# Performance work log

Measured on AMD Instinct MI355X. Metric: run time of the kernel, lower is better.

The kernel has to match this reference:

```python
import jax, jax.numpy as jnp
import numpy as np

B, T, C, H, HS = 4, 2048, 1024, 16, 64
EPS = 1e-5


def setup_inputs() -> dict:
    key = jax.random.key(0)
    ks = jax.random.split(key, 16)
    s = lambda k, shp, fan: jax.random.normal(k, shp, jnp.float32) * (fan ** -0.5)
    return {
        "x": jax.random.normal(ks[0], (B, T, C), jnp.float32),
        "wq": s(ks[1], (H, C, HS), C), "bq": jnp.zeros((H, HS), jnp.float32),
        "wk": s(ks[2], (H, C, HS), C), "bk": jnp.zeros((H, HS), jnp.float32),
        "wv": s(ks[3], (H, C, HS), C), "bv": jnp.zeros((H, HS), jnp.float32),
        "wp": s(ks[4], (C, C), C), "bp": jnp.zeros((C,), jnp.float32),
        "w1": s(ks[5], (C, 4 * C), C), "b1": jnp.zeros((4 * C,), jnp.float32),
        "w2": s(ks[6], (4 * C, C), 4 * C), "b2": jnp.zeros((C,), jnp.float32),
        "g1": jnp.ones((C,), jnp.float32), "be1": jnp.zeros((C,), jnp.float32),
        "g2": jnp.ones((C,), jnp.float32), "be2": jnp.zeros((C,), jnp.float32),
    }


def _layernorm(x, g, b):
    mu = jnp.mean(x, axis=-1, keepdims=True)
    var = jnp.mean(jnp.square(x - mu), axis=-1, keepdims=True)
    return (x - mu) * jax.lax.rsqrt(var + EPS) * g + b


def reference(x, wq, bq, wk, bk, wv, bv, wp, bp, w1, b1, w2, b2, g1, be1, g2, be2):
    Bc, Tc, Cc = x.shape
    h = _layernorm(x, g1, be1)
    # per-head projections stacked: [B,H,T,HS]
    q = jnp.einsum('btc,hcd->bhtd', h, wq) + bq[None, :, None, :]
    k = jnp.einsum('btc,hcd->bhtd', h, wk) + bk[None, :, None, :]
    v = jnp.einsum('btc,hcd->bhtd', h, wv) + bv[None, :, None, :]
    # NOTE: source scales by 1/sqrt(n_embd), not 1/sqrt(head_size)
    scores = jnp.einsum('bhtd,bhsd->bhts', q, k) * (Cc ** -0.5)
    causal = jnp.tril(jnp.ones((Tc, Tc), bool))
    scores = jnp.where(causal, scores, -jnp.inf)
    attn = jax.nn.softmax(scores, axis=-1)
    out = jnp.einsum('bhts,bhsd->bhtd', attn, v)
    out = out.transpose(0, 2, 1, 3).reshape(Bc, Tc, Cc)  # concat heads
    x = x + out @ wp + bp
    h2 = _layernorm(x, g2, be2)
    ffn = jax.nn.relu(h2 @ w1 + b1) @ w2 + b2
    return x + ffn
```

## Files before the change

kernel.cpp:

```cpp
#include <hip/hip_runtime.h>


constexpr int Bb = 4, Tt = 2048, Cc = 1024, Hh = 16, HSz = 64, Ff = 4096;
constexpr int Mrows = Bb * Tt;

typedef __attribute__((ext_vector_type(8))) short bf16x8;
typedef __attribute__((ext_vector_type(4))) float f32x4;

__device__ __forceinline__ ushort f2bf(float f) {
  uint u = __builtin_bit_cast(uint, f);
  uint r = (u + 0x7fffu + ((u >> 16) & 1u)) >> 16;
  return (ushort)r;
}
__device__ __forceinline__ float bf2f(ushort s) {
  return __builtin_bit_cast(float, ((uint)s) << 16);
}
__device__ __forceinline__ uint cvtpk_bf16(float lo, float hi) {
  uint r;
  asm("v_cvt_pk_bf16_f32 %0, %1, %2" : "=v"(r) : "v"(lo), "v"(hi));
  return r;
}
__device__ __forceinline__ void gload16(const void* g, void* l) {
  __builtin_amdgcn_global_load_lds(
      (const __attribute__((address_space(1))) void*)g,
      (__attribute__((address_space(3))) void*)l, 16, 0, 0);
}

__global__ __launch_bounds__(256) void ln_kernel(const float* __restrict__ x,
                                                 const float* __restrict__ g,
                                                 const float* __restrict__ b,
                                                 ushort* __restrict__ out) {
  int row = blockIdx.x;
  const float* xr = x + (size_t)row * Cc;
  int c4 = threadIdx.x * 4;
  float4 v = *(const float4*)(xr + c4);
  float s1 = v.x + v.y + v.z + v.w;
  float s2 = v.x * v.x + v.y * v.y + v.z * v.z + v.w * v.w;
#pragma unroll
  for (int off = 32; off >= 1; off >>= 1) {
    s1 += __shfl_xor(s1, off);
    s2 += __shfl_xor(s2, off);
  }
  __shared__ float red[8];
  int wid = threadIdx.x >> 6, lane = threadIdx.x & 63;
  if (lane == 0) { red[wid] = s1; red[4 + wid] = s2; }
  __syncthreads();
  float t1 = red[0] + red[1] + red[2] + red[3];
  float t2 = red[4] + red[5] + red[6] + red[7];
  float mu = t1 * (1.0f / Cc);
  float var = t2 * (1.0f / Cc) - mu * mu;
  float rs = rsqrtf(var + 1e-5f);
  float4 gv = *(const float4*)(g + c4);
  float4 bv = *(const float4*)(b + c4);
  ushort4 o;
  o.x = f2bf((v.x - mu) * rs * gv.x + bv.x);
  o.y = f2bf((v.y - mu) * rs * gv.y + bv.y);
  o.z = f2bf((v.z - mu) * rs * gv.z + bv.z);
  o.w = f2bf((v.w - mu) * rs * gv.w + bv.w);
  *(ushort4*)(out + (size_t)row * Cc + c4) = o;
}

__device__ __forceinline__ void tcast_body(const float* __restrict__ src,
                                           ushort* __restrict__ dst, int ldS,
                                           int ldD, int r0, int c0) {
  __shared__ float t[32][33];
  int c = threadIdx.x & 31, r8 = threadIdx.x >> 5;
#pragma unroll
  for (int i = 0; i < 4; ++i) {
    int r = r8 + i * 8;
    t[r][c] = src[(size_t)(r0 + r) * ldS + c0 + c];
  }
  __syncthreads();
#pragma unroll
  for (int i = 0; i < 4; ++i) {
    int rr = r8 + i * 8;
    dst[(size_t)(c0 + rr) * ldD + r0 + c] = f2bf(t[c][rr]);
  }
}

__global__ __launch_bounds__(256) void tcast_kernel(const float* __restrict__ src,
                                                    ushort* __restrict__ dst,
                                                    int ldS, int ldD) {
  tcast_body(src, dst, ldS, ldD, blockIdx.x * 32, blockIdx.y * 32);
}

__global__ __launch_bounds__(256) void tcast_qkv(const float* __restrict__ wq,
                                                 const float* __restrict__ wk,
                                                 const float* __restrict__ wv,
                                                 ushort* __restrict__ dst) {
  int z = blockIdx.z, zz = z >> 4, h = z & 15;
  const float* src = (zz == 0 ? wq : (zz == 1 ? wk : wv)) + (size_t)h * Cc * HSz;
  ushort* d = dst + (size_t)(zz * 1024 + h * 64) * 1024;
  tcast_body(src, d, HSz, Cc, blockIdx.x * 32, blockIdx.y * 32);
}

__global__ __launch_bounds__(256) void bias_concat(const float* __restrict__ bq,
                                                   const float* __restrict__ bk,
                                                   const float* __restrict__ bv,
                                                   float* __restrict__ dst) {
  int i = blockIdx.x * 256 + threadIdx.x;
  dst[i] = i < 1024 ? bq[i] : (i < 2048 ? bk[i - 1024] : bv[i - 2048]);
}

__device__ __forceinline__ void gemm_main(const ushort* __restrict__ A, int lda,
                                          const ushort* __restrict__ Bt, int ldb,
                                          int K, int m0, int n0,
                                          ushort* __restrict__ As,
                                          ushort* __restrict__ Bs,
                                          f32x4 (&acc)[4][2]) {
  int tid = threadIdx.x, wid = tid >> 6, lane = tid & 63;
  int wr = wid >> 2, wc = wid & 3, fr = lane & 15, fq = lane >> 4;
  const ushort* Ag = A + (size_t)m0 * lda;
  const ushort* Bg = Bt + (size_t)n0 * ldb;
  for (int k0 = 0; k0 < K; k0 += 64) {
#pragma unroll
    for (int c = 0; c < 2; ++c) {
      int slot = c * 512 + tid;
      int row = slot >> 3, s = slot & 7;
      int sw = (s << 3) ^ ((row & 7) << 3);
      gload16(Ag + (size_t)row * lda + k0 + sw, As + (size_t)(c * 512 + wid * 64) * 8);
      gload16(Bg + (size_t)row * ldb + k0 + sw, Bs + (size_t)(c * 512 + wid * 64) * 8);
    }
    __syncthreads();
    bf16x8 av[4][2], bv[2][2];
#pragma unroll
    for (int m = 0; m < 4; ++m) {
      int row = wr * 64 + m * 16 + fr;
#pragma unroll
      for (int ks = 0; ks < 2; ++ks)
        av[m][ks] = *(const bf16x8*)&As[row * 64 + (((ks * 4 + fq) ^ (row & 7)) << 3)];
    }
#pragma unroll
    for (int n = 0; n < 2; ++n) {
      int row = wc * 32 + n * 16 + fr;
#pragma unroll
      for (int ks = 0; ks < 2; ++ks)
        bv[n][ks] = *(const bf16x8*)&Bs[row * 64 + (((ks * 4 + fq) ^ (row & 7)) << 3)];
    }
#pragma unroll
    for (int m = 0; m < 4; ++m)
#pragma unroll
      for (int n = 0; n < 2; ++n)
#pragma unroll
        for (int ks = 0; ks < 2; ++ks)
          acc[m][n] = __builtin_amdgcn_mfma_f32_16x16x32_bf16(
              av[m][ks], bv[n][ks], acc[m][n], 0, 0, 0);
    __syncthreads();
  }
}

__device__ __forceinline__ void xcd_swz(int& bx, int& by) {
  int bid = blockIdx.x + blockIdx.y * gridDim.x;
  int cpx = (gridDim.x * gridDim.y) >> 3;
  int id = (bid & 7) * cpx + (bid >> 3);
  bx = id % gridDim.x;
  by = id / gridDim.x;
}

template <bool RELU, bool HASRES, bool OUTBF16>
__global__ __launch_bounds__(512) void gemm_bf16(
    const ushort* __restrict__ A, int lda, const ushort* __restrict__ Bt,
    int ldb, const float* __restrict__ bias, const float* __restrict__ res,
    void* __restrict__ Cout, int ldc, int K) {
  __shared__ __align__(16) ushort As[128 * 64];
  __shared__ __align__(16) ushort Bs[128 * 64];
  f32x4 acc[4][2] = {};
  int bx, by;
  xcd_swz(bx, by);
  int m0 = by * 128, n0 = bx * 128;
  gemm_main(A, lda, Bt, ldb, K, m0, n0, As, Bs, acc);
  int lane = threadIdx.x & 63, wid = threadIdx.x >> 6;
  int wr = wid >> 2, wc = wid & 3, fr = lane & 15, fq = lane >> 4;
#pragma unroll
  for (int m = 0; m < 4; ++m) {
    int gm = m0 + wr * 64 + m * 16 + fq * 4;
#pragma unroll
    for (int n = 0; n < 2; ++n) {
      int gn = n0 + wc * 32 + n * 16 + fr;
      float bsv = bias[gn];
#pragma unroll
      for (int j = 0; j < 4; ++j) {
        int row = gm + j;
        float v = acc[m][n][j] + bsv;
        if constexpr (HASRES) v += res[(size_t)row * ldc + gn];
        if constexpr (RELU) v = fmaxf(v, 0.f);
        if constexpr (OUTBF16)
          ((ushort*)Cout)[(size_t)row * ldc + gn] = f2bf(v);
        else
          ((float*)Cout)[(size_t)row * ldc + gn] = v;
      }
    }
  }
}

__global__ __launch_bounds__(512) void gemm_qkv(const ushort* __restrict__ A,
                                                const ushort* __restrict__ Bt,
                                                const float* __restrict__ bias,
                                                ushort* __restrict__ q,
                                                ushort* __restrict__ k,
                                                ushort* __restrict__ vt) {
  __shared__ __align__(16) ushort As[128 * 64];
  __shared__ __align__(16) ushort Bs[128 * 64];
  f32x4 acc[4][2] = {};
  int bx, by;
  xcd_swz(bx, by);
  int m0 = by * 128, n0 = bx * 128;
  gemm_main(A, 1024, Bt, 1024, 1024, m0, n0, As, Bs, acc);
  int lane = threadIdx.x & 63, wid = threadIdx.x >> 6;
  int wr = wid >> 2, wc = wid & 3, fr = lane & 15, fq = lane >> 4;
  const float qscale = 1.4426950408889634f / 32.0f;
#pragma unroll
  for (int m = 0; m < 4; ++m) {
    int gm = m0 + wr * 64 + m * 16 + fq * 4;
#pragma unroll
    for (int n = 0; n < 2; ++n) {
      int gn = n0 + wc * 32 + n * 16 + fr;
      float bsv = bias[gn];
      if (gn < 1024) {
#pragma unroll
        for (int j = 0; j < 4; ++j)
          q[(size_t)(gm + j) * 1024 + gn] = f2bf((acc[m][n][j] + bsv) * qscale);
      } else if (gn < 2048) {
        int col = gn - 1024;
#pragma unroll
        for (int j = 0; j < 4; ++j)
          k[(size_t)(gm + j) * 1024 + col] = f2bf(acc[m][n][j] + bsv);
      } else {
        int dd = gn - 2048, h = dd >> 6, d = dd & 63;
        int bbr = gm >> 11, t = gm & 2047;
        ushort4 pw = {f2bf(acc[m][n][0] + bsv), f2bf(acc[m][n][1] + bsv),
                      f2bf(acc[m][n][2] + bsv), f2bf(acc[m][n][3] + bsv)};
        *(ushort4*)&vt[(((size_t)(bbr * 16 + h)) * 64 + d) * 2048 + t] = pw;
      }
    }
  }
}

constexpr int QB = 128, KVB = 64;
__global__ __launch_bounds__(256) void attn_kernel(const ushort* __restrict__ Qb,
                                                   const ushort* __restrict__ Kb,
                                                   const ushort* __restrict__ Vt,
                                                   ushort* __restrict__ att) {
  __shared__ __align__(16) ushort Klds[64 * 64];
  __shared__ __align__(16) ushort Vlds[64 * 64];
  __shared__ __align__(16) ushort Plds[4][32 * 64];
  int tid = threadIdx.x, wid = tid >> 6, lane = tid & 63;
  int fr = lane & 15, fq = lane >> 4;
  int bh = blockIdx.y, bb = bh >> 4, hh = bh & 15;
  const ushort* qkbase = Qb + ((size_t)bb * Tt) * Cc + hh * HSz;
  const ushort* Kbase = Kb + ((size_t)bb * Tt) * Cc + hh * HSz;
  const ushort* Vbase = Vt + ((size_t)(bb * Hh + hh)) * HSz * Tt;

#pragma unroll 1
  for (int pass = 0; pass < 2; ++pass) {
    int qt = pass ? (Tt / QB - 1 - (int)blockIdx.x) : (int)blockIdx.x;
    int q0 = qt * QB;
    int q0w = q0 + wid * 32;

    bf16x8 Qreg[2][2];
#pragma unroll
    for (int qs = 0; qs < 2; ++qs)
#pragma unroll
      for (int d2 = 0; d2 < 2; ++d2)
        Qreg[qs][d2] = *(const bf16x8*)(qkbase +
            (size_t)(q0w + qs * 16 + fr) * Cc + d2 * 32 + fq * 8);
    f32x4 Oa[2][4] = {};
    float mrow[2] = {-1e30f, -1e30f}, lrow[2] = {0.f, 0.f};
    int nt = q0 / KVB + 2;

    for (int kt = 0; kt < nt; ++kt) {
      int t0 = kt * KVB;
      __syncthreads();
#pragma unroll
      for (int cch = 0; cch < 2; ++cch) {
        int s = cch * 256 + tid;
        int row = s >> 3;
        int b = (s & 7) * 16;
        int sw = (b >> 1) ^ ((row & 7) << 3);
        void* dst = (char*)Klds + (cch * 256 + wid * 64) * 16;
        gload16(Kbase + (size_t)(t0 + row) * Cc + sw, dst);
        void* dstv = (char*)Vlds + (cch * 256 + wid * 64) * 16;
        gload16(Vbase + (size_t)row * Tt + t0 + sw, dstv);
      }
      __syncthreads();
      if (q0w + 31 < t0) continue;

      bf16x8 kf[4][2];
#pragma unroll
      for (int ks = 0; ks < 4; ++ks)
#pragma unroll
        for (int d2 = 0; d2 < 2; ++d2) {
          int row = ks * 16 + fr;
          int off = (d2 * 64 + fq * 16) ^ ((row & 7) << 4);
          kf[ks][d2] = *(const bf16x8*)((const char*)Klds + row * 128 + off);
        }
      f32x4 accs[2][4] = {};
      __builtin_amdgcn_s_setprio(1);
#pragma unroll
      for (int qs = 0; qs < 2; ++qs)
#pragma unroll
        for (int ks = 0; ks < 4; ++ks) {
          accs[qs][ks] = __builtin_amdgcn_mfma_f32_16x16x32_bf16(
              kf[ks][0], Qreg[qs][0], accs[qs][ks], 0, 0, 0);
          accs[qs][ks] = __builtin_amdgcn_mfma_f32_16x16x32_bf16(
              kf[ks][1], Qreg[qs][1], accs[qs][ks], 0, 0, 0);
        }
      __builtin_amdgcn_s_setprio(0);

#pragma unroll
      for (int qs = 0; qs < 2; ++qs) {
        float sv[4][4];
        float vmax = -1e30f;
        if (t0 + 63 <= q0w + qs * 16) {
#pragma unroll
          for (int ks = 0; ks < 4; ++ks)
#pragma unroll
            for (int j = 0; j < 4; ++j) {
              sv[ks][j] = accs[qs][ks][j];
              vmax = fmaxf(vmax, sv[ks][j]);
            }
        } else {
          int qg = q0w + qs * 16 + fr;
#pragma unroll
          for (int ks = 0; ks < 4; ++ks)
#pragma unroll
            for (int j = 0; j < 4; ++j) {
              int kg = t0 + ks * 16 + fq * 4 + j;
              float s = accs[qs][ks][j];
              s = (kg <= qg) ? s : -1e30f;
              sv[ks][j] = s;
              vmax = fmaxf(vmax, s);
            }
        }
        vmax = fmaxf(vmax, __shfl_xor(vmax, 16));
        vmax = fmaxf(vmax, __shfl_xor(vmax, 32));
        float mnew = mrow[qs];
        if (!__all(vmax <= mnew + 11.0f)) {
          mnew = fmaxf(mrow[qs], vmax);
          float sf = exp2f(mrow[qs] - mnew);
          mrow[qs] = mnew;
          lrow[qs] *= sf;
#pragma unroll
          for (int j = 0; j < 4; ++j) {
            float sfo = __shfl(sf, fq * 4 + j);
#pragma unroll
            for (int ds = 0; ds < 4; ++ds) Oa[qs][ds][j] *= sfo;
          }
        }
        float ls = 0.f;
        int qrow = qs * 16 + fr;
        char* pbase = (char*)Plds[wid] + qrow * 128;
#pragma unroll
        for (int ks = 0; ks < 4; ++ks) {
          float p0 = exp2f(sv[ks][0] - mnew);
          float p1 = exp2f(sv[ks][1] - mnew);
          float p2 = exp2f(sv[ks][2] - mnew);
          float p3 = exp2f(sv[ks][3] - mnew);
          ls += (p0 + p1) + (p2 + p3);
          uint2 pw = {cvtpk_bf16(p0, p1), cvtpk_bf16(p2, p3)};
          int off = (ks * 32 + fq * 8) ^ ((qrow & 7) << 4);
          *(uint2*)(pbase + off) = pw;
        }
        ls += __shfl_xor(ls, 16);
        ls += __shfl_xor(ls, 32);
        lrow[qs] += ls;
      }

      bf16x8 vf[4][2];
#pragma unroll
      for (int ds = 0; ds < 4; ++ds)
#pragma unroll
        for (int k2 = 0; k2 < 2; ++k2) {
          int row = ds * 16 + fr;
          int off = (k2 * 64 + fq * 16) ^ ((row & 7) << 4);
          vf[ds][k2] = *(const bf16x8*)((const char*)Vlds + row * 128 + off);
        }
      __builtin_amdgcn_s_setprio(1);
#pragma unroll
      for (int qs = 0; qs < 2; ++qs) {
        int qrow = qs * 16 + fr;
        bf16x8 pf[2];
#pragma unroll
        for (int k2 = 0; k2 < 2; ++k2) {
          int off = (k2 * 64 + fq * 16) ^ ((qrow & 7) << 4);
          pf[k2] = *(const bf16x8*)((const char*)Plds[wid] + qrow * 128 + off);
        }
#pragma unroll
        for (int ds = 0; ds < 4; ++ds) {
          Oa[qs][ds] = __builtin_amdgcn_mfma_f32_16x16x32_bf16(
              pf[0], vf[ds][0], Oa[qs][ds], 0, 0, 0);
          Oa[qs][ds] = __builtin_amdgcn_mfma_f32_16x16x32_bf16(
              pf[1], vf[ds][1], Oa[qs][ds], 0, 0, 0);
        }
      }
      __builtin_amdgcn_s_setprio(0);
    }

#pragma unroll
    for (int qs = 0; qs < 2; ++qs) {
      float linv = 1.f / lrow[qs];
#pragma unroll
      for (int j = 0; j < 4; ++j) {
        float lo = __shfl(linv, fq * 4 + j);
        int qg = q0w + qs * 16 + fq * 4 + j;
        ushort* orow = att + (size_t)(bb * Tt + qg) * Cc + hh * HSz;
#pragma unroll
        for (int ds = 0; ds < 4; ++ds)
          orow[ds * 16 + fr] = f2bf(Oa[qs][ds][j] * lo);
      }
    }
  }
}

extern "C" void kernel_launch(void* const* d_in, const int* in_sizes, int n_in,
                              void* d_out, int out_size, void* d_ws,
                              size_t ws_size, hipStream_t stream) {
  const float* x = (const float*)d_in[0];
  const float* wq = (const float*)d_in[1];
  const float* bq = (const float*)d_in[2];
  const float* wk = (const float*)d_in[3];
  const float* bk = (const float*)d_in[4];
  const float* wv = (const float*)d_in[5];
  const float* bv = (const float*)d_in[6];
  const float* wp = (const float*)d_in[7];
  const float* bp = (const float*)d_in[8];
  const float* w1 = (const float*)d_in[9];
  const float* b1 = (const float*)d_in[10];
  const float* w2 = (const float*)d_in[11];
  const float* b2 = (const float*)d_in[12];
  const float* g1 = (const float*)d_in[13];
  const float* be1 = (const float*)d_in[14];
  const float* g2 = (const float*)d_in[15];
  const float* be2 = (const float*)d_in[16];
  float* out = (float*)d_out;

  ushort* Qb = (ushort*)d_ws;
  ushort* Kb = Qb + (size_t)8388608;
  ushort* Vt = Kb + (size_t)8388608;
  ushort* att = Vt + (size_t)8388608;
  ushort* ffh = Qb;
  ushort* h1b = att + (size_t)8388608;
  float* x2 = (float*)(h1b + (size_t)8388608);
  ushort* wqkvT = (ushort*)(x2 + (size_t)8388608);
  ushort* wpT = wqkvT + (size_t)3145728;
  ushort* w1T = wpT + (size_t)1048576;
  ushort* w2T = w1T + (size_t)4194304;
  float* bqkv = (float*)(w2T + (size_t)4194304);

  tcast_qkv<<<dim3(32, 2, 48), 256, 0, stream>>>(wq, wk, wv, wqkvT);
  tcast_kernel<<<dim3(32, 32), 256, 0, stream>>>(wp, wpT, 1024, 1024);
  tcast_kernel<<<dim3(32, 128), 256, 0, stream>>>(w1, w1T, 4096, 1024);
  tcast_kernel<<<dim3(128, 32), 256, 0, stream>>>(w2, w2T, 1024, 4096);
  bias_concat<<<dim3(12), 256, 0, stream>>>(bq, bk, bv, bqkv);

  ln_kernel<<<dim3(Mrows), 256, 0, stream>>>(x, g1, be1, h1b);
  gemm_qkv<<<dim3(24, 64), 512, 0, stream>>>(h1b, wqkvT, bqkv, Qb, Kb, Vt);
  attn_kernel<<<dim3(Tt / QB / 2, Bb * Hh), 256, 0, stream>>>(Qb, Kb, Vt, att);
  gemm_bf16<false, true, false><<<dim3(8, 64), 512, 0, stream>>>(
      att, 1024, wpT, 1024, bp, x, x2, 1024, 1024);
  ln_kernel<<<dim3(Mrows), 256, 0, stream>>>(x2, g2, be2, h1b);
  gemm_bf16<true, false, true><<<dim3(32, 64), 512, 0, stream>>>(
      h1b, 1024, w1T, 1024, b1, nullptr, ffh, 4096, 1024);
  gemm_bf16<false, true, false><<<dim3(8, 64), 512, 0, stream>>>(
      ffh, 4096, w2T, 4096, b2, x2, out, 1024, 4096);
}
```

Baseline: 384.0 us.

## Split attention query tile across 8 waves of 16 rows each

```diff
diff --git a/kernel.cpp b/kernel.cpp
--- a/kernel.cpp
+++ b/kernel.cpp
@@ -237,13 +237,13 @@
 }
 
 constexpr int QB = 128, KVB = 64;
-__global__ __launch_bounds__(256) void attn_kernel(const ushort* __restrict__ Qb,
+__global__ __launch_bounds__(512) void attn_kernel(const ushort* __restrict__ Qb,
                                                    const ushort* __restrict__ Kb,
                                                    const ushort* __restrict__ Vt,
                                                    ushort* __restrict__ att) {
   __shared__ __align__(16) ushort Klds[64 * 64];
   __shared__ __align__(16) ushort Vlds[64 * 64];
-  __shared__ __align__(16) ushort Plds[4][32 * 64];
+  __shared__ __align__(16) ushort Plds[8][16 * 64];
   int tid = threadIdx.x, wid = tid >> 6, lane = tid & 63;
   int fr = lane & 15, fq = lane >> 4;
   int bh = blockIdx.y, bb = bh >> 4, hh = bh & 15;
@@ -255,35 +255,28 @@
   for (int pass = 0; pass < 2; ++pass) {
     int qt = pass ? (Tt / QB - 1 - (int)blockIdx.x) : (int)blockIdx.x;
     int q0 = qt * QB;
-    int q0w = q0 + wid * 32;
-
-    bf16x8 Qreg[2][2];
-#pragma unroll
-    for (int qs = 0; qs < 2; ++qs)
-#pragma unroll
-      for (int d2 = 0; d2 < 2; ++d2)
-        Qreg[qs][d2] = *(const bf16x8*)(qkbase +
-            (size_t)(q0w + qs * 16 + fr) * Cc + d2 * 32 + fq * 8);
-    f32x4 Oa[2][4] = {};
-    float mrow[2] = {-1e30f, -1e30f}, lrow[2] = {0.f, 0.f};
+    int q0w = q0 + wid * 16;
+
+    bf16x8 Qreg[2];
+#pragma unroll
+    for (int d2 = 0; d2 < 2; ++d2)
+      Qreg[d2] = *(const bf16x8*)(qkbase + (size_t)(q0w + fr) * Cc + d2 * 32 + fq * 8);
+    f32x4 Oa[4] = {};
+    float mrow = -1e30f, lrow = 0.f;
     int nt = q0 / KVB + 2;
 
     for (int kt = 0; kt < nt; ++kt) {
       int t0 = kt * KVB;
       __syncthreads();
-#pragma unroll
-      for (int cch = 0; cch < 2; ++cch) {
-        int s = cch * 256 + tid;
-        int row = s >> 3;
-        int b = (s & 7) * 16;
+      {
+        int row = tid >> 3;
+        int b = (tid & 7) * 16;
         int sw = (b >> 1) ^ ((row & 7) << 3);
-        void* dst = (char*)Klds + (cch * 256 + wid * 64) * 16;
-        gload16(Kbase + (size_t)(t0 + row) * Cc + sw, dst);
-        void* dstv = (char*)Vlds + (cch * 256 + wid * 64) * 16;
-        gload16(Vbase + (size_t)row * Tt + t0 + sw, dstv);
+        gload16(Kbase + (size_t)(t0 + row) * Cc + sw, (char*)Klds + wid * 1024);
+        gload16(Vbase + (size_t)row * Tt + t0 + sw, (char*)Vlds + wid * 1024);
       }
       __syncthreads();
-      if (q0w + 31 < t0) continue;
+      if (q0w + 15 < t0) continue;
 
       bf16x8 kf[4][2];
 #pragma unroll
@@ -294,77 +287,71 @@
           int off = (d2 * 64 + fq * 16) ^ ((row & 7) << 4);
           kf[ks][d2] = *(const bf16x8*)((const char*)Klds + row * 128 + off);
         }
-      f32x4 accs[2][4] = {};
+      f32x4 accs[4] = {};
       __builtin_amdgcn_s_setprio(1);
 #pragma unroll
-      for (int qs = 0; qs < 2; ++qs)
-#pragma unroll
-        for (int ks = 0; ks < 4; ++ks) {
-          accs[qs][ks] = __builtin_amdgcn_mfma_f32_16x16x32_bf16(
-              kf[ks][0], Qreg[qs][0], accs[qs][ks], 0, 0, 0);
-          accs[qs][ks] = __builtin_amdgcn_mfma_f32_16x16x32_bf16(
-              kf[ks][1], Qreg[qs][1], accs[qs][ks], 0, 0, 0);
+      for (int ks = 0; ks < 4; ++ks) {
+        accs[ks] = __builtin_amdgcn_mfma_f32_16x16x32_bf16(
+            kf[ks][0], Qreg[0], accs[ks], 0, 0, 0);
+        accs[ks] = __builtin_amdgcn_mfma_f32_16x16x32_bf16(
+            kf[ks][1], Qreg[1], accs[ks], 0, 0, 0);
+      }
+      __builtin_amdgcn_s_setprio(0);
+
+      float sv[4][4];
+      float vmax = -1e30f;
+      if (t0 + 63 <= q0w) {
+#pragma unroll
+        for (int ks = 0; ks < 4; ++ks)
+#pragma unroll
+          for (int j = 0; j < 4; ++j) {
+            sv[ks][j] = accs[ks][j];
+            vmax = fmaxf(vmax, sv[ks][j]);
+          }
+      } else {
+        int qg = q0w + fr;
+#pragma unroll
+        for (int ks = 0; ks < 4; ++ks)
+#pragma unroll
+          for (int j = 0; j < 4; ++j) {
+            int kg = t0 + ks * 16 + fq * 4 + j;
+            float s = accs[ks][j];
+            s = (kg <= qg) ? s : -1e30f;
+            sv[ks][j] = s;
+            vmax = fmaxf(vmax, s);
+          }
+      }
+      vmax = fmaxf(vmax, __shfl_xor(vmax, 16));
+      vmax = fmaxf(vmax, __shfl_xor(vmax, 32));
+      float mnew = mrow;
+      if (!__all(vmax <= mnew + 11.0f)) {
+        mnew = fmaxf(mrow, vmax);
+        float sf = exp2f(mrow - mnew);
+        mrow = mnew;
+        lrow *= sf;
+#pragma unroll
+        for (int j = 0; j < 4; ++j) {
+          float sfo = __shfl(sf, fq * 4 + j);
+#pragma unroll
+          for (int ds = 0; ds < 4; ++ds) Oa[ds][j] *= sfo;
         }
-      __builtin_amdgcn_s_setprio(0);
-
-#pragma unroll
-      for (int qs = 0; qs < 2; ++qs) {
-        float sv[4][4];
-        float vmax = -1e30f;
-        if (t0 + 63 <= q0w + qs * 16) {
-#pragma unroll
-          for (int ks = 0; ks < 4; ++ks)
-#pragma unroll
-            for (int j = 0; j < 4; ++j) {
-              sv[ks][j] = accs[qs][ks][j];
-              vmax = fmaxf(vmax, sv[ks][j]);
-            }
-        } else {
-          int qg = q0w + qs * 16 + fr;
-#pragma unroll
-          for (int ks = 0; ks < 4; ++ks)
-#pragma unroll
-            for (int j = 0; j < 4; ++j) {
-              int kg = t0 + ks * 16 + fq * 4 + j;
-              float s = accs[qs][ks][j];
-              s = (kg <= qg) ? s : -1e30f;
-              sv[ks][j] = s;
-              vmax = fmaxf(vmax, s);
-            }
-        }
-        vmax = fmaxf(vmax, __shfl_xor(vmax, 16));
-        vmax = fmaxf(vmax, __shfl_xor(vmax, 32));
-        float mnew = mrow[qs];
-        if (!__all(vmax <= mnew + 11.0f)) {
-          mnew = fmaxf(mrow[qs], vmax);
-          float sf = exp2f(mrow[qs] - mnew);
-          mrow[qs] = mnew;
-          lrow[qs] *= sf;
-#pragma unroll
-          for (int j = 0; j < 4; ++j) {
-            float sfo = __shfl(sf, fq * 4 + j);
-#pragma unroll
-            for (int ds = 0; ds < 4; ++ds) Oa[qs][ds][j] *= sfo;
-          }
-        }
-        float ls = 0.f;
-        int qrow = qs * 16 + fr;
-        char* pbase = (char*)Plds[wid] + qrow * 128;
-#pragma unroll
-        for (int ks = 0; ks < 4; ++ks) {
-          float p0 = exp2f(sv[ks][0] - mnew);
-          float p1 = exp2f(sv[ks][1] - mnew);
-          float p2 = exp2f(sv[ks][2] - mnew);
-          float p3 = exp2f(sv[ks][3] - mnew);
-          ls += (p0 + p1) + (p2 + p3);
-          uint2 pw = {cvtpk_bf16(p0, p1), cvtpk_bf16(p2, p3)};
-          int off = (ks * 32 + fq * 8) ^ ((qrow & 7) << 4);
-          *(uint2*)(pbase + off) = pw;
-        }
-        ls += __shfl_xor(ls, 16);
-        ls += __shfl_xor(ls, 32);
-        lrow[qs] += ls;
-      }
+      }
+      float ls = 0.f;
+      char* pbase = (char*)Plds[wid] + fr * 128;
+#pragma unroll
+      for (int ks = 0; ks < 4; ++ks) {
+        float p0 = exp2f(sv[ks][0] - mnew);
+        float p1 = exp2f(sv[ks][1] - mnew);
+        float p2 = exp2f(sv[ks][2] - mnew);
+        float p3 = exp2f(sv[ks][3] - mnew);
+        ls += (p0 + p1) + (p2 + p3);
+        uint2 pw = {cvtpk_bf16(p0, p1), cvtpk_bf16(p2, p3)};
+        int off = (ks * 32 + fq * 8) ^ ((fr & 7) << 4);
+        *(uint2*)(pbase + off) = pw;
+      }
+      ls += __shfl_xor(ls, 16);
+      ls += __shfl_xor(ls, 32);
+      lrow += ls;
 
       bf16x8 vf[4][2];
 #pragma unroll
@@ -375,38 +362,33 @@
           int off = (k2 * 64 + fq * 16) ^ ((row & 7) << 4);
           vf[ds][k2] = *(const bf16x8*)((const char*)Vlds + row * 128 + off);
         }
+      bf16x8 pf[2];
+#pragma unroll
+      for (int k2 = 0; k2 < 2; ++k2) {
+        int off = (k2 * 64 + fq * 16) ^ ((fr & 7) << 4);
+        pf[k2] = *(const bf16x8*)((const char*)Plds[wid] + fr * 128 + off);
+      }
       __builtin_amdgcn_s_setprio(1);
 #pragma unroll
-      for (int qs = 0; qs < 2; ++qs) {
-        int qrow = qs * 16 + fr;
-        bf16x8 pf[2];
-#pragma unroll
-        for (int k2 = 0; k2 < 2; ++k2) {
-          int off = (k2 * 64 + fq * 16) ^ ((qrow & 7) << 4);
-          pf[k2] = *(const bf16x8*)((const char*)Plds[wid] + qrow * 128 + off);
-        }
-#pragma unroll
-        for (int ds = 0; ds < 4; ++ds) {
-          Oa[qs][ds] = __builtin_amdgcn_mfma_f32_16x16x32_bf16(
-              pf[0], vf[ds][0], Oa[qs][ds], 0, 0, 0);
-          Oa[qs][ds] = __builtin_amdgcn_mfma_f32_16x16x32_bf16(
-              pf[1], vf[ds][1], Oa[qs][ds], 0, 0, 0);
-        }
+      for (int ds = 0; ds < 4; ++ds) {
+        Oa[ds] = __builtin_amdgcn_mfma_f32_16x16x32_bf16(
+            pf[0], vf[ds][0], Oa[ds], 0, 0, 0);
+        Oa[ds] = __builtin_amdgcn_mfma_f32_16x16x32_bf16(
+            pf[1], vf[ds][1], Oa[ds], 0, 0, 0);
       }
       __builtin_amdgcn_s_setprio(0);
     }
 
-#pragma unroll
-    for (int qs = 0; qs < 2; ++qs) {
-      float linv = 1.f / lrow[qs];
+    {
+      float linv = 1.f / lrow;
 #pragma unroll
       for (int j = 0; j < 4; ++j) {
         float lo = __shfl(linv, fq * 4 + j);
-        int qg = q0w + qs * 16 + fq * 4 + j;
+        int qg = q0w + fq * 4 + j;
         ushort* orow = att + (size_t)(bb * Tt + qg) * Cc + hh * HSz;
 #pragma unroll
         for (int ds = 0; ds < 4; ++ds)
-          orow[ds * 16 + fr] = f2bf(Oa[qs][ds][j] * lo);
+          orow[ds * 16 + fr] = f2bf(Oa[ds][j] * lo);
       }
     }
   }
@@ -455,7 +437,7 @@
 
   ln_kernel<<<dim3(Mrows), 256, 0, stream>>>(x, g1, be1, h1b);
   gemm_qkv<<<dim3(24, 64), 512, 0, stream>>>(h1b, wqkvT, bqkv, Qb, Kb, Vt);
-  attn_kernel<<<dim3(Tt / QB / 2, Bb * Hh), 256, 0, stream>>>(Qb, Kb, Vt, att);
+  attn_kernel<<<dim3(Tt / QB / 2, Bb * Hh), 512, 0, stream>>>(Qb, Kb, Vt, att);
   gemm_bf16<false, true, false><<<dim3(8, 64), 512, 0, stream>>>(
       att, 1024, wpT, 1024, bp, x, x2, 1024, 1024);
   ln_kernel<<<dim3(Mrows), 256, 0, stream>>>(x2, g2, be2, h1b);
```

After: 370.9 us. -3.4%, faster.
